# Kernel tuning notes

Hardware: AMD Instinct MI355X
Metric: run time of the kernel (lower is better)

The kernel has to match this reference:

```python
import jax, jax.numpy as jnp
import numpy as np

N = 50000          # num nodes
E = 800000         # num edges (before self loops)
DIM_IN = 128
HID = 32           # per-head hidden of conv1
HEADS = 8          # heads of conv1
DIM_OUT = 16       # output classes (conv2, 1 head, concat=False)
NEG_SLOPE = 0.2    # GATConv default leaky_relu slope


def gat_conv(x, W, a_src, a_dst, bias, src, dst, heads, out_ch, concat):
    """PyG GATConv (self-loops already appended to src/dst).
    x: [N, F_in], W: [F_in, heads*out_ch], a_src/a_dst: [heads, out_ch], bias matches output.
    """
    n = x.shape[0]
    h = (x @ W).reshape(n, heads, out_ch)                    # [N, H, C]
    al_src = jnp.einsum('nhc,hc->nh', h, a_src)              # [N, H]
    al_dst = jnp.einsum('nhc,hc->nh', h, a_dst)              # [N, H]
    e = jax.nn.leaky_relu(al_src[src] + al_dst[dst], NEG_SLOPE)   # [E', H]
    # segment softmax over edges grouped by target node (dst)
    emax = jax.ops.segment_max(e, dst, num_segments=n)       # [N, H]
    ee = jnp.exp(e - emax[dst])                              # [E', H]
    denom = jax.ops.segment_sum(ee, dst, num_segments=n)     # [N, H]
    alpha = ee / (denom[dst] + 1e-16)                        # [E', H]
    msg = h[src] * alpha[:, :, None]                         # [E', H, C]
    out = jax.ops.segment_sum(msg, dst, num_segments=n)      # [N, H, C]
    out = out.reshape(n, heads * out_ch) if concat else out.mean(axis=1)
    return out + bias


def setup_inputs() -> dict:
    key = jax.random.key(0)
    ks = jax.random.split(key, 12)
    x = jax.random.normal(ks[0], (N, DIM_IN), dtype=jnp.float32)
    edge_index = jax.random.randint(ks[1], (2, E), 0, N, dtype=jnp.int64)
    s = 0.1
    W1 = jax.random.normal(ks[2], (DIM_IN, HEADS * HID), dtype=jnp.float32) * s
    a1_src = jax.random.normal(ks[3], (HEADS, HID), dtype=jnp.float32) * s
    a1_dst = jax.random.normal(ks[4], (HEADS, HID), dtype=jnp.float32) * s
    b1 = jnp.zeros((HEADS * HID,), dtype=jnp.float32)
    W2 = jax.random.normal(ks[5], (HEADS * HID, DIM_OUT), dtype=jnp.float32) * s
    a2_src = jax.random.normal(ks[6], (1, DIM_OUT), dtype=jnp.float32) * s
    a2_dst = jax.random.normal(ks[7], (1, DIM_OUT), dtype=jnp.float32) * s
    b2 = jnp.zeros((DIM_OUT,), dtype=jnp.float32)
    return {"x": x, "edge_index": edge_index, "W1": W1, "a1_src": a1_src,
            "a1_dst": a1_dst, "b1": b1, "W2": W2, "a2_src": a2_src,
            "a2_dst": a2_dst, "b2": b2}


def reference(x, edge_index, W1, a1_src, a1_dst, b1, W2, a2_src, a2_dst, b2):
    # add self loops (GATConv default add_self_loops=True)
    loops = jnp.arange(N, dtype=edge_index.dtype)
    src = jnp.concatenate([edge_index[0], loops])
    dst = jnp.concatenate([edge_index[1], loops])
    # dropout layers are identity in eval mode
    h = gat_conv(x, W1, a1_src, a1_dst, b1, src, dst, HEADS, HID, concat=True)
    h = jax.nn.elu(h)
    out = gat_conv(h, W2, a2_src, a2_dst, b2, src, dst, 1, DIM_OUT, concat=False)
    return jax.nn.log_softmax(out, axis=1)
```

## Files before the change

kernel.cpp:

```cpp
#include <hip/hip_runtime.h>
#include <hip/hip_bf16.h>

#define NN 50000
#define EE 800000
#define EP (EE + NN)
#define DIN 128
#define HID 32
#define HEADS 8
#define C1 (HEADS * HID)
#define DOUT 16
#define NW1 3125
#define SH 9
#define NB 98
#define CAP 16384
#define EPT 8
#define BBLK (256 * EPT)
#define GB1 196

typedef __attribute__((ext_vector_type(8))) short short8;
typedef __attribute__((ext_vector_type(4))) float float4v;
typedef __attribute__((ext_vector_type(2))) float float2v;

__device__ inline unsigned short f2bf(float f) {
    __hip_bfloat16 b = __float2bfloat16(f);
    return *reinterpret_cast<unsigned short*>(&b);
}
__device__ inline float bflo(unsigned u) {
    union { unsigned int i; float f; } x;
    x.i = u << 16;
    return x.f;
}
__device__ inline float bfhi(unsigned u) {
    union { unsigned int i; float f; } x;
    x.i = u & 0xffff0000u;
    return x.f;
}
__device__ inline float bf2f(unsigned short u) {
    union { unsigned int i; float f; } x;
    x.i = ((unsigned int)u) << 16;
    return x.f;
}

__global__ void k_prepfw(const float* __restrict__ W1, const float* __restrict__ a1s,
                         const float* __restrict__ a1d, const float* __restrict__ W2,
                         unsigned short* __restrict__ w1frag,
                         unsigned short* __restrict__ w2frag,
                         int* __restrict__ cntb) {
    int i = blockIdx.x * 256 + threadIdx.x;
    if (blockIdx.x == 0 && threadIdx.x < NB) cntb[threadIdx.x] = 0;
    if (i < 17 * 2048) {
        int j = i & 7, lane = (i >> 3) & 63, s = (i >> 9) & 3, c = i >> 11;
        int q = lane >> 4, m = lane & 15;
        int k = s * 32 + q * 8 + j;
        float val;
        if (c < 16) {
            val = W1[k * C1 + c * 16 + m];
        } else {
            int h = m & 7;
            const float* av = (m < 8) ? a1s : a1d;
            float acc = 0.f;
            #pragma unroll
            for (int j2 = 0; j2 < 32; j2++)
                acc += W1[k * C1 + h * 32 + j2] * av[h * 32 + j2];
            val = acc;
        }
        w1frag[i] = f2bf(val);
    } else if (i < 17 * 2048 + 8 * 512) {
        int j2 = i - 17 * 2048;
        int jj = j2 & 7, lane = (j2 >> 3) & 63, s = j2 >> 9;
        int q = lane >> 4, m = lane & 15;
        w2frag[j2] = f2bf(W2[(s * 32 + q * 8 + jj) * DOUT + m]);
    }
}

__global__ __launch_bounds__(256) void k_bucketA(const int* __restrict__ ei,
                                                 int* __restrict__ cntb,
                                                 unsigned* __restrict__ ebuf) {
    __shared__ int hist[4][NB];
    __shared__ int base[4][NB];
    int t = threadIdx.x;
    int wave = t >> 6;
    for (int i = t; i < 4 * NB; i += 256) ((int*)hist)[i] = 0;
    __syncthreads();
    int e0 = blockIdx.x * BBLK;
    int s[EPT], d[EPT], r[EPT];
    #pragma unroll
    for (int j = 0; j < EPT; j++) {
        int e = e0 + j * 256 + t;
        int ss = 0, dd = -1;
        if (e < EE) { ss = ei[e]; dd = ei[EE + e]; }
        else if (e < EP) { ss = e - EE; dd = ss; }
        s[j] = ss; d[j] = dd;
        if (dd >= 0) r[j] = atomicAdd(&hist[wave][dd >> SH], 1);
    }
    __syncthreads();
    if (t < NB) {
        int h0 = hist[0][t], h1 = hist[1][t], h2 = hist[2][t], h3 = hist[3][t];
        int tot = h0 + h1 + h2 + h3;
        int bb = tot ? atomicAdd(&cntb[t], tot) : 0;
        base[0][t] = bb;
        base[1][t] = bb + h0;
        base[2][t] = bb + h0 + h1;
        base[3][t] = bb + h0 + h1 + h2;
    }
    __syncthreads();
    #pragma unroll
    for (int j = 0; j < EPT; j++) {
        if (d[j] >= 0) {
            int b = d[j] >> SH;
            ebuf[b * CAP + base[wave][b] + r[j]] =
                ((unsigned)s[j] << SH) | (unsigned)(d[j] & 511);
        }
    }
}

__global__ __launch_bounds__(1024) void k_csrgemm1(const int* __restrict__ cntb,
                                                   const unsigned* __restrict__ ebuf,
                                                   int* __restrict__ row_ptr,
                                                   int* __restrict__ esrc,
                                                   const float* __restrict__ x,
                                                   const unsigned short* __restrict__ w1frag,
                                                   unsigned char* __restrict__ h1f8,
                                                   float* __restrict__ al1sd,
                                                   unsigned short* __restrict__ al1s8) {
    __shared__ int sdeg[512];
    __shared__ int wtot[8];
    __shared__ int bpart[2];
    if (blockIdx.x < NB) {
        int b = blockIdx.x;
        int t = threadIdx.x;
        int lane = t & 63, wave = t >> 6;
        int nodes0 = b << SH;
        if (t < 512) sdeg[t] = 0;
        if (t < 128) {
            int v = (t < b) ? cntb[t] : 0;
            #pragma unroll
            for (int off = 1; off < 64; off <<= 1) v += __shfl_xor(v, off, 64);
            if (lane == 0) bpart[wave] = v;
        }
        __syncthreads();
        int baseS = bpart[0] + bpart[1];
        int cnt = cntb[b];
        const unsigned* eb = ebuf + b * CAP;
        for (int i = t; i < cnt; i += 1024)
            atomicAdd(&sdeg[eb[i] & 511], 1);
        __syncthreads();
        int v = (t < 512) ? sdeg[t] : 0;
        int inc = v;
        #pragma unroll
        for (int off = 1; off < 64; off <<= 1) {
            int u = __shfl_up(inc, off, 64);
            if (lane >= off) inc += u;
        }
        if (t < 512 && lane == 63) wtot[wave] = inc;
        __syncthreads();
        if (wave == 0 && lane < 8) {
            int w = wtot[lane];
            int iw = w;
            #pragma unroll
            for (int off = 1; off < 8; off <<= 1) {
                int u = __shfl_up(iw, off, 64);
                if (lane >= off) iw += u;
            }
            wtot[lane] = iw - w;
        }
        __syncthreads();
        int excl = inc - v + ((t < 512) ? wtot[wave] : 0);
        __syncthreads();
        if (t < 512) {
            sdeg[t] = excl;
            int node = nodes0 + t;
            if (node < NN) row_ptr[node] = baseS + excl;
        }
        __syncthreads();
        for (int i = t; i < cnt; i += 1024) {
            unsigned e = eb[i];
            int pos = atomicAdd(&sdeg[e & 511], 1);
            esrc[baseS + pos] = (int)(e >> SH);
        }
        if (b == 0 && t == 0) row_ptr[NN] = EP;
    } else {
        int wid = (blockIdx.x - NB) * 16 + (threadIdx.x >> 6);
        int lane = threadIdx.x & 63;
        if (wid >= NW1) return;
        int nb = wid * 16;
        int m = lane & 15, quad = lane >> 4;
        const float* xrow = x + (nb + m) * DIN;

        short8 bfr[4];
        #pragma unroll
        for (int s = 0; s < 4; s++) {
            float4 f0 = *(const float4*)(xrow + s * 32 + quad * 8);
            float4 f1 = *(const float4*)(xrow + s * 32 + quad * 8 + 4);
            unsigned short* bp = (unsigned short*)&bfr[s];
            bp[0] = f2bf(f0.x); bp[1] = f2bf(f0.y); bp[2] = f2bf(f0.z); bp[3] = f2bf(f0.w);
            bp[4] = f2bf(f1.x); bp[5] = f2bf(f1.y); bp[6] = f2bf(f1.z); bp[7] = f2bf(f1.w);
        }

        float4v acc[17];
        #pragma unroll
        for (int c = 0; c < 17; c++) acc[c] = (float4v){0.f, 0.f, 0.f, 0.f};

        #pragma unroll
        for (int s = 0; s < 4; s++) {
            const unsigned short* fp = w1frag + (s * 64 + lane) * 8;
            #pragma unroll
            for (int c = 0; c < 17; c++) {
                short8 afrag = *(const short8*)(fp + c * 2048);
                acc[c] = __builtin_amdgcn_mfma_f32_16x16x32_bf16(afrag, bfr[s], acc[c], 0, 0, 0);
            }
        }

        int node = nb + m;
        #pragma unroll
        for (int c = 0; c < 16; c++) {
            unsigned pk = 0;
            pk = __builtin_amdgcn_cvt_pk_fp8_f32(acc[c][0], acc[c][1], pk, false);
            pk = __builtin_amdgcn_cvt_pk_fp8_f32(acc[c][2], acc[c][3], pk, true);
            *(unsigned*)(h1f8 + node * C1 + c * 16 + quad * 4) = pk;
        }
        *(float4*)(al1sd + node * 16 + quad * 4) =
            make_float4(acc[16][0], acc[16][1], acc[16][2], acc[16][3]);
        if (quad < 2) {
            uint2 pk;
            pk.x = (unsigned)f2bf(acc[16][0]) | ((unsigned)f2bf(acc[16][1]) << 16);
            pk.y = (unsigned)f2bf(acc[16][2]) | ((unsigned)f2bf(acc[16][3]) << 16);
            *(uint2*)(al1s8 + node * 8 + quad * 4) = pk;
        }
    }
}

__global__ __launch_bounds__(256) void k_agg1(const int* __restrict__ row_ptr,
                                              const int* __restrict__ esrc,
                                              const unsigned char* __restrict__ h1f8,
                                              const unsigned short* __restrict__ al1s8,
                                              const float* __restrict__ al1sd,
                                              const float* __restrict__ b1,
                                              unsigned short* __restrict__ helu_b) {
    __shared__ float wbuf[4][64 * 8];
    __shared__ int   sbuf[4][64];
    int wslot = threadIdx.x >> 6;
    int L = threadIdx.x & 63;
    int d = (blockIdx.x * 256 + threadIdx.x) >> 6;
    int h = L >> 3;
    int start = row_ptr[d], end = row_ptr[d + 1];
    float4 ald0 = *(const float4*)(al1sd + d * 16 + 8);
    float4 ald1 = *(const float4*)(al1sd + d * 16 + 12);
    float* wrow = wbuf[wslot];
    int* srow = sbuf[wslot];
    float denom = 0.f;
    float4 acc = make_float4(0.f, 0.f, 0.f, 0.f);
    const int Lofs = L * 4;

    for (int base = start; base < end; base += 64) {
        int cnt = min(64, end - base);
        int s = d;
        float wv0 = 0.f, wv1 = 0.f, wv2 = 0.f, wv3 = 0.f;
        float wv4 = 0.f, wv5 = 0.f, wv6 = 0.f, wv7 = 0.f;
        if (L < cnt) {
            s = esrc[base + L];
            uint4 as = *(const uint4*)(al1s8 + s * 8);
            float e;
            e = bflo(as.x) + ald0.x; e = e > 0.f ? e : 0.2f * e; wv0 = __expf(e);
            e = bfhi(as.x) + ald0.y; e = e > 0.f ? e : 0.2f * e; wv1 = __expf(e);
            e = bflo(as.y) + ald0.z; e = e > 0.f ? e : 0.2f * e; wv2 = __expf(e);
            e = bfhi(as.y) + ald0.w; e = e > 0.f ? e : 0.2f * e; wv3 = __expf(e);
            e = bflo(as.z) + ald1.x; e = e > 0.f ? e : 0.2f * e; wv4 = __expf(e);
            e = bfhi(as.z) + ald1.y; e = e > 0.f ? e : 0.2f * e; wv5 = __expf(e);
            e = bflo(as.w) + ald1.z; e = e > 0.f ? e : 0.2f * e; wv6 = __expf(e);
            e = bfhi(as.w) + ald1.w; e = e > 0.f ? e : 0.2f * e; wv7 = __expf(e);
        }
        srow[L] = s;
        *(float4*)&wrow[L * 8]     = make_float4(wv0, wv1, wv2, wv3);
        *(float4*)&wrow[L * 8 + 4] = make_float4(wv4, wv5, wv6, wv7);
        int cnt4 = (cnt + 3) & ~3;
        for (int i = 0; i < cnt4; i += 4) {
            int s0 = srow[i], s1 = srow[i + 1], s2 = srow[i + 2], s3 = srow[i + 3];
            float x0 = wrow[i * 8 + h];
            float x1 = wrow[i * 8 + 8 + h];
            float x2 = wrow[i * 8 + 16 + h];
            float x3 = wrow[i * 8 + 24 + h];
            unsigned v0 = *(const unsigned*)(h1f8 + s0 * C1 + Lofs);
            unsigned v1 = *(const unsigned*)(h1f8 + s1 * C1 + Lofs);
            unsigned v2 = *(const unsigned*)(h1f8 + s2 * C1 + Lofs);
            unsigned v3 = *(const unsigned*)(h1f8 + s3 * C1 + Lofs);
            denom += (x0 + x1) + (x2 + x3);
            float2v a, b;
            a = __builtin_amdgcn_cvt_pk_f32_fp8(v0, false);
            b = __builtin_amdgcn_cvt_pk_f32_fp8(v0, true);
            acc.x += x0 * a.x; acc.y += x0 * a.y; acc.z += x0 * b.x; acc.w += x0 * b.y;
            a = __builtin_amdgcn_cvt_pk_f32_fp8(v1, false);
            b = __builtin_amdgcn_cvt_pk_f32_fp8(v1, true);
            acc.x += x1 * a.x; acc.y += x1 * a.y; acc.z += x1 * b.x; acc.w += x1 * b.y;
            a = __builtin_amdgcn_cvt_pk_f32_fp8(v2, false);
            b = __builtin_amdgcn_cvt_pk_f32_fp8(v2, true);
            acc.x += x2 * a.x; acc.y += x2 * a.y; acc.z += x2 * b.x; acc.w += x2 * b.y;
            a = __builtin_amdgcn_cvt_pk_f32_fp8(v3, false);
            b = __builtin_amdgcn_cvt_pk_f32_fp8(v3, true);
            acc.x += x3 * a.x; acc.y += x3 * a.y; acc.z += x3 * b.x; acc.w += x3 * b.y;
        }
    }
    float inv = 1.0f / (denom + 1e-16f);
    float4 bv = *(const float4*)(b1 + Lofs);
    float o0 = acc.x * inv + bv.x;
    float o1 = acc.y * inv + bv.y;
    float o2 = acc.z * inv + bv.z;
    float o3 = acc.w * inv + bv.w;
    o0 = o0 > 0.f ? o0 : __expf(o0) - 1.0f;
    o1 = o1 > 0.f ? o1 : __expf(o1) - 1.0f;
    o2 = o2 > 0.f ? o2 : __expf(o2) - 1.0f;
    o3 = o3 > 0.f ? o3 : __expf(o3) - 1.0f;
    uint2 pk;
    pk.x = (unsigned)f2bf(o0) | ((unsigned)f2bf(o1) << 16);
    pk.y = (unsigned)f2bf(o2) | ((unsigned)f2bf(o3) << 16);
    *(uint2*)(helu_b + d * C1 + Lofs) = pk;
}

__global__ __launch_bounds__(256) void k_gemm2(const unsigned short* __restrict__ helu_b,
                                               const unsigned short* __restrict__ w2frag,
                                               const float* __restrict__ a2s,
                                               const float* __restrict__ a2d,
                                               unsigned short* __restrict__ h2b,
                                               float* __restrict__ al2s,
                                               float* __restrict__ al2d) {
    int wid = (blockIdx.x * 256 + threadIdx.x) >> 6;
    int lane = threadIdx.x & 63;
    int nb = wid * 16;
    if (nb >= NN) return;
    int m = lane & 15, quad = lane >> 4;

    const unsigned short* wp2 = w2frag + lane * 8;
    float4v acc = {0.f, 0.f, 0.f, 0.f};
    const unsigned short* arow = helu_b + (nb + m) * C1 + quad * 8;
    #pragma unroll
    for (int s = 0; s < 8; s++) {
        short8 afrag = *(const short8*)(arow + s * 32);
        short8 bfrag = *(const short8*)(wp2 + s * 512);
        acc = __builtin_amdgcn_mfma_f32_16x16x32_bf16(afrag, bfrag, acc, 0, 0, 0);
    }

    float as_c = a2s[m], ad_c = a2d[m];
    #pragma unroll
    for (int r = 0; r < 4; r++) {
        int node = nb + quad * 4 + r;
        float val = acc[r];
        h2b[node * DOUT + m] = f2bf(val);
        float ps = val * as_c;
        float pd = val * ad_c;
        ps += __shfl_xor(ps, 1, 64); ps += __shfl_xor(ps, 2, 64);
        ps += __shfl_xor(ps, 4, 64); ps += __shfl_xor(ps, 8, 64);
        pd += __shfl_xor(pd, 1, 64); pd += __shfl_xor(pd, 2, 64);
        pd += __shfl_xor(pd, 4, 64); pd += __shfl_xor(pd, 8, 64);
        if (m == 0) {
            al2s[node] = ps;
            al2d[node] = pd;
        }
    }
}

__global__ __launch_bounds__(256) void k_agg2(const int* __restrict__ row_ptr,
                                              const int* __restrict__ esrc,
                                              const unsigned short* __restrict__ h2b,
                                              const float* __restrict__ al2s,
                                              const float* __restrict__ al2d,
                                              const float* __restrict__ b2,
                                              float* __restrict__ out) {
    __shared__ float wbuf2[4][64];
    __shared__ int   sbuf2[4][64];
    int wslot = threadIdx.x >> 6;
    int L = threadIdx.x & 63;
    int n = (blockIdx.x * 256 + threadIdx.x) >> 6;
    if (n >= NN) return;
    int c = L & 15, g = L >> 4;
    int start = row_ptr[n], end = row_ptr[n + 1];
    float ald = al2d[n];
    float* wrow = wbuf2[wslot];
    int* srow = sbuf2[wslot];
    float acc = 0.f, denom = 0.f;

    for (int base = start; base < end; base += 64) {
        int cnt = min(64, end - base);
        int s = n; float w = 0.f;
        if (L < cnt) {
            s = esrc[base + L];
            float e = al2s[s] + ald;
            e = e > 0.f ? e : 0.2f * e;
            w = __expf(e);
        }
        srow[L] = s;
        wrow[L] = w;
        int cnt4 = (cnt + 3) & ~3;
        for (int i = 0; i < cnt4; i += 4) {
            int idx = i + g;
            int ss = srow[idx];
            float ww = wrow[idx];
            float v = bf2f(h2b[ss * DOUT + c]);
            acc += ww * v;
            denom += ww;
        }
    }
    acc += __shfl_xor(acc, 16, 64);   acc += __shfl_xor(acc, 32, 64);
    denom += __shfl_xor(denom, 16, 64); denom += __shfl_xor(denom, 32, 64);
    float val = acc / (denom + 1e-16f) + b2[c];
    float m = val;
    #pragma unroll
    for (int mm = 1; mm < 16; mm <<= 1) m = fmaxf(m, __shfl_xor(m, mm, 64));
    float ex = __expf(val - m);
    float se = ex;
    #pragma unroll
    for (int mm = 1; mm < 16; mm <<= 1) se += __shfl_xor(se, mm, 64);
    if (L < 16) out[n * DOUT + c] = val - m - __logf(se);
}

extern "C" void kernel_launch(void* const* d_in, const int* in_sizes, int n_in,
                              void* d_out, int out_size, void* d_ws, size_t ws_size,
                              hipStream_t stream) {
    const float* x   = (const float*)d_in[0];
    const int*   ei  = (const int*)d_in[1];
    const float* W1  = (const float*)d_in[2];
    const float* a1s = (const float*)d_in[3];
    const float* a1d = (const float*)d_in[4];
    const float* b1  = (const float*)d_in[5];
    const float* W2  = (const float*)d_in[6];
    const float* a2s = (const float*)d_in[7];
    const float* a2d = (const float*)d_in[8];
    const float* b2  = (const float*)d_in[9];
    float* outp = (float*)d_out;

    unsigned char* h1f8    = (unsigned char*)d_ws;
    unsigned short* helu_b = (unsigned short*)(h1f8 + NN * C1);
    unsigned short* h2b    = helu_b + NN * C1;
    unsigned short* w2frag = h2b + NN * DOUT;
    unsigned short* w1frag = w2frag + 8 * 512;
    unsigned short* al1s8  = w1frag + 17 * 2048;
    float* al1sd = (float*)(al1s8 + NN * 8);
    float* al2sb = al1sd + NN * 16;
    float* al2db = al2sb + NN;
    int* row_ptr = (int*)(al2db + NN);
    int* esrc    = row_ptr + NN + 1;
    int* cntb    = esrc + EP;
    unsigned* ebuf = (unsigned*)helu_b;

    k_prepfw<<<(17 * 2048 + 8 * 512 + 255) / 256, 256, 0, stream>>>(W1, a1s, a1d, W2, w1frag, w2frag, cntb);
    k_bucketA<<<(EP + BBLK - 1) / BBLK, 256, 0, stream>>>(ei, cntb, ebuf);
    k_csrgemm1<<<NB + GB1, 1024, 0, stream>>>(cntb, ebuf, row_ptr, esrc,
                                              x, w1frag, h1f8, al1sd, al1s8);
    k_agg1<<<12500, 256, 0, stream>>>(row_ptr, esrc, h1f8, al1s8, al1sd, b1, helu_b);
    k_gemm2<<<(NW1 * 64 + 255) / 256, 256, 0, stream>>>(helu_b, w2frag, a2s, a2d, h2b, al2sb, al2db);
    k_agg2<<<(NN * 64 + 255) / 256, 256, 0, stream>>>(row_ptr, esrc, h2b, al2sb, al2db, b2, outp);
}
```

Baseline: 215.4 us.

## Split fused CSR/GEMM1 kernel and widen agg2 per-lane feature loads

Splits the combined CSR-build and first GEMM kernel into two launches: a 256-thread GEMM kernel with x loads hoisted ahead of the bf16 conversion, followed by a 1024-thread CSR kernel. This should give the GEMM better occupancy than it had inside 1024-thread blocks. In agg2, each lane now reads two bf16 features at once, so 8 edges are processed per iteration instead of 4, and the log-softmax uses one reciprocal and float2 stores. The cost is an extra kernel launch, and the CSR and GEMM phases can no longer run at the same time within one grid.

```diff
diff --git a/kernel.cpp b/kernel.cpp
--- a/kernel.cpp
+++ b/kernel.cpp
@@ -15,7 +15,6 @@
 #define CAP 16384
 #define EPT 8
 #define BBLK (256 * EPT)
-#define GB1 196
 
 typedef __attribute__((ext_vector_type(8))) short short8;
 typedef __attribute__((ext_vector_type(4))) float float4v;
@@ -114,119 +113,123 @@
     }
 }
 
-__global__ __launch_bounds__(1024) void k_csrgemm1(const int* __restrict__ cntb,
-                                                   const unsigned* __restrict__ ebuf,
-                                                   int* __restrict__ row_ptr,
-                                                   int* __restrict__ esrc,
-                                                   const float* __restrict__ x,
-                                                   const unsigned short* __restrict__ w1frag,
-                                                   unsigned char* __restrict__ h1f8,
-                                                   float* __restrict__ al1sd,
-                                                   unsigned short* __restrict__ al1s8) {
+__global__ __launch_bounds__(1024) void k_csr(const int* __restrict__ cntb,
+                                              const unsigned* __restrict__ ebuf,
+                                              int* __restrict__ row_ptr,
+                                              int* __restrict__ esrc) {
     __shared__ int sdeg[512];
     __shared__ int wtot[8];
     __shared__ int bpart[2];
-    if (blockIdx.x < NB) {
-        int b = blockIdx.x;
-        int t = threadIdx.x;
-        int lane = t & 63, wave = t >> 6;
-        int nodes0 = b << SH;
-        if (t < 512) sdeg[t] = 0;
-        if (t < 128) {
-            int v = (t < b) ? cntb[t] : 0;
-            #pragma unroll
-            for (int off = 1; off < 64; off <<= 1) v += __shfl_xor(v, off, 64);
-            if (lane == 0) bpart[wave] = v;
-        }
-        __syncthreads();
-        int baseS = bpart[0] + bpart[1];
-        int cnt = cntb[b];
-        const unsigned* eb = ebuf + b * CAP;
-        for (int i = t; i < cnt; i += 1024)
-            atomicAdd(&sdeg[eb[i] & 511], 1);
-        __syncthreads();
-        int v = (t < 512) ? sdeg[t] : 0;
-        int inc = v;
+    int b = blockIdx.x;
+    int t = threadIdx.x;
+    int lane = t & 63, wave = t >> 6;
+    int nodes0 = b << SH;
+    if (t < 512) sdeg[t] = 0;
+    if (t < 128) {
+        int v = (t < b) ? cntb[t] : 0;
         #pragma unroll
-        for (int off = 1; off < 64; off <<= 1) {
-            int u = __shfl_up(inc, off, 64);
-            if (lane >= off) inc += u;
-        }
-        if (t < 512 && lane == 63) wtot[wave] = inc;
-        __syncthreads();
-        if (wave == 0 && lane < 8) {
-            int w = wtot[lane];
-            int iw = w;
-            #pragma unroll
-            for (int off = 1; off < 8; off <<= 1) {
-                int u = __shfl_up(iw, off, 64);
-                if (lane >= off) iw += u;
-            }
-            wtot[lane] = iw - w;
-        }
-        __syncthreads();
-        int excl = inc - v + ((t < 512) ? wtot[wave] : 0);
-        __syncthreads();
-        if (t < 512) {
-            sdeg[t] = excl;
-            int node = nodes0 + t;
-            if (node < NN) row_ptr[node] = baseS + excl;
-        }
-        __syncthreads();
-        for (int i = t; i < cnt; i += 1024) {
-            unsigned e = eb[i];
-            int pos = atomicAdd(&sdeg[e & 511], 1);
-            esrc[baseS + pos] = (int)(e >> SH);
-        }
-        if (b == 0 && t == 0) row_ptr[NN] = EP;
-    } else {
-        int wid = (blockIdx.x - NB) * 16 + (threadIdx.x >> 6);
-        int lane = threadIdx.x & 63;
-        if (wid >= NW1) return;
-        int nb = wid * 16;
-        int m = lane & 15, quad = lane >> 4;
-        const float* xrow = x + (nb + m) * DIN;
-
-        short8 bfr[4];
+        for (int off = 1; off < 64; off <<= 1) v += __shfl_xor(v, off, 64);
+        if (lane == 0) bpart[wave] = v;
+    }
+    __syncthreads();
+    int baseS = bpart[0] + bpart[1];
+    int cnt = cntb[b];
+    const unsigned* eb = ebuf + b * CAP;
+    for (int i = t; i < cnt; i += 1024)
+        atomicAdd(&sdeg[eb[i] & 511], 1);
+    __syncthreads();
+    int v = (t < 512) ? sdeg[t] : 0;
+    int inc = v;
+    #pragma unroll
+    for (int off = 1; off < 64; off <<= 1) {
+        int u = __shfl_up(inc, off, 64);
+        if (lane >= off) inc += u;
+    }
+    if (t < 512 && lane == 63) wtot[wave] = inc;
+    __syncthreads();
+    if (wave == 0 && lane < 8) {
+        int w = wtot[lane];
+        int iw = w;
         #pragma unroll
-        for (int s = 0; s < 4; s++) {
-            float4 f0 = *(const float4*)(xrow + s * 32 + quad * 8);
-            float4 f1 = *(const float4*)(xrow + s * 32 + quad * 8 + 4);
-            unsigned short* bp = (unsigned short*)&bfr[s];
-            bp[0] = f2bf(f0.x); bp[1] = f2bf(f0.y); bp[2] = f2bf(f0.z); bp[3] = f2bf(f0.w);
-            bp[4] = f2bf(f1.x); bp[5] = f2bf(f1.y); bp[6] = f2bf(f1.z); bp[7] = f2bf(f1.w);
-        }
-
-        float4v acc[17];
+        for (int off = 1; off < 8; off <<= 1) {
+            int u = __shfl_up(iw, off, 64);
+            if (lane >= off) iw += u;
+        }
+        wtot[lane] = iw - w;
+    }
+    __syncthreads();
+    int excl = inc - v + ((t < 512) ? wtot[wave] : 0);
+    __syncthreads();
+    if (t < 512) {
+        sdeg[t] = excl;
+        int node = nodes0 + t;
+        if (node < NN) row_ptr[node] = baseS + excl;
+    }
+    __syncthreads();
+    for (int i = t; i < cnt; i += 1024) {
+        unsigned e = eb[i];
+        int pos = atomicAdd(&sdeg[e & 511], 1);
+        esrc[baseS + pos] = (int)(e >> SH);
+    }
+    if (b == 0 && t == 0) row_ptr[NN] = EP;
+}
+
+__global__ __launch_bounds__(256) void k_gemm1(const float* __restrict__ x,
+                                               const unsigned short* __restrict__ w1frag,
+                                               unsigned char* __restrict__ h1f8,
+                                               float* __restrict__ al1sd,
+                                               unsigned short* __restrict__ al1s8) {
+    int wid = (blockIdx.x * 256 + threadIdx.x) >> 6;
+    int lane = threadIdx.x & 63;
+    if (wid >= NW1) return;
+    int nb = wid * 16;
+    int m = lane & 15, quad = lane >> 4;
+    const float* xrow = x + (nb + m) * DIN;
+
+    float4 xf[8];
+    #pragma unroll
+    for (int s = 0; s < 4; s++) {
+        xf[2 * s]     = *(const float4*)(xrow + s * 32 + quad * 8);
+        xf[2 * s + 1] = *(const float4*)(xrow + s * 32 + quad * 8 + 4);
+    }
+    short8 bfr[4];
+    #pragma unroll
+    for (int s = 0; s < 4; s++) {
+        unsigned short* bp = (unsigned short*)&bfr[s];
+        float4 f0 = xf[2 * s], f1 = xf[2 * s + 1];
+        bp[0] = f2bf(f0.x); bp[1] = f2bf(f0.y); bp[2] = f2bf(f0.z); bp[3] = f2bf(f0.w);
+        bp[4] = f2bf(f1.x); bp[5] = f2bf(f1.y); bp[6] = f2bf(f1.z); bp[7] = f2bf(f1.w);
+    }
+
+    float4v acc[17];
+    #pragma unroll
+    for (int c = 0; c < 17; c++) acc[c] = (float4v){0.f, 0.f, 0.f, 0.f};
+
+    #pragma unroll
+    for (int s = 0; s < 4; s++) {
+        const unsigned short* fp = w1frag + (s * 64 + lane) * 8;
         #pragma unroll
-        for (int c = 0; c < 17; c++) acc[c] = (float4v){0.f, 0.f, 0.f, 0.f};
-
-        #pragma unroll
-        for (int s = 0; s < 4; s++) {
-            const unsigned short* fp = w1frag + (s * 64 + lane) * 8;
-            #pragma unroll
-            for (int c = 0; c < 17; c++) {
-                short8 afrag = *(const short8*)(fp + c * 2048);
-                acc[c] = __builtin_amdgcn_mfma_f32_16x16x32_bf16(afrag, bfr[s], acc[c], 0, 0, 0);
-            }
-        }
-
-        int node = nb + m;
-        #pragma unroll
-        for (int c = 0; c < 16; c++) {
-            unsigned pk = 0;
-            pk = __builtin_amdgcn_cvt_pk_fp8_f32(acc[c][0], acc[c][1], pk, false);
-            pk = __builtin_amdgcn_cvt_pk_fp8_f32(acc[c][2], acc[c][3], pk, true);
-            *(unsigned*)(h1f8 + node * C1 + c * 16 + quad * 4) = pk;
-        }
-        *(float4*)(al1sd + node * 16 + quad * 4) =
-            make_float4(acc[16][0], acc[16][1], acc[16][2], acc[16][3]);
-        if (quad < 2) {
-            uint2 pk;
-            pk.x = (unsigned)f2bf(acc[16][0]) | ((unsigned)f2bf(acc[16][1]) << 16);
-            pk.y = (unsigned)f2bf(acc[16][2]) | ((unsigned)f2bf(acc[16][3]) << 16);
-            *(uint2*)(al1s8 + node * 8 + quad * 4) = pk;
-        }
+        for (int c = 0; c < 17; c++) {
+            short8 afrag = *(const short8*)(fp + c * 2048);
+            acc[c] = __builtin_amdgcn_mfma_f32_16x16x32_bf16(afrag, bfr[s], acc[c], 0, 0, 0);
+        }
+    }
+
+    int node = nb + m;
+    #pragma unroll
+    for (int c = 0; c < 16; c++) {
+        unsigned pk = 0;
+        pk = __builtin_amdgcn_cvt_pk_fp8_f32(acc[c][0], acc[c][1], pk, false);
+        pk = __builtin_amdgcn_cvt_pk_fp8_f32(acc[c][2], acc[c][3], pk, true);
+        *(unsigned*)(h1f8 + node * C1 + c * 16 + quad * 4) = pk;
+    }
+    *(float4*)(al1sd + node * 16 + quad * 4) =
+        make_float4(acc[16][0], acc[16][1], acc[16][2], acc[16][3]);
+    if (quad < 2) {
+        uint2 pk;
+        pk.x = (unsigned)f2bf(acc[16][0]) | ((unsigned)f2bf(acc[16][1]) << 16);
+        pk.y = (unsigned)f2bf(acc[16][2]) | ((unsigned)f2bf(acc[16][3]) << 16);
+        *(uint2*)(al1s8 + node * 8 + quad * 4) = pk;
     }
 }
 
@@ -371,12 +374,12 @@
     int L = threadIdx.x & 63;
     int n = (blockIdx.x * 256 + threadIdx.x) >> 6;
     if (n >= NN) return;
-    int c = L & 15, g = L >> 4;
+    int p = L & 7, g = L >> 3;
     int start = row_ptr[n], end = row_ptr[n + 1];
     float ald = al2d[n];
     float* wrow = wbuf2[wslot];
     int* srow = sbuf2[wslot];
-    float acc = 0.f, denom = 0.f;
+    float acc0 = 0.f, acc1 = 0.f, denom = 0.f;
 
     for (int base = start; base < end; base += 64) {
         int cnt = min(64, end - base);
@@ -389,27 +392,35 @@
         }
         srow[L] = s;
         wrow[L] = w;
-        int cnt4 = (cnt + 3) & ~3;
-        for (int i = 0; i < cnt4; i += 4) {
+        int cnt8 = (cnt + 7) & ~7;
+        for (int i = 0; i < cnt8; i += 8) {
             int idx = i + g;
             int ss = srow[idx];
             float ww = wrow[idx];
-            float v = bf2f(h2b[ss * DOUT + c]);
-            acc += ww * v;
+            unsigned v = *(const unsigned*)(h2b + ss * DOUT + p * 2);
+            acc0 += ww * bflo(v);
+            acc1 += ww * bfhi(v);
             denom += ww;
         }
     }
-    acc += __shfl_xor(acc, 16, 64);   acc += __shfl_xor(acc, 32, 64);
-    denom += __shfl_xor(denom, 16, 64); denom += __shfl_xor(denom, 32, 64);
-    float val = acc / (denom + 1e-16f) + b2[c];
-    float m = val;
-    #pragma unroll
-    for (int mm = 1; mm < 16; mm <<= 1) m = fmaxf(m, __shfl_xor(m, mm, 64));
-    float ex = __expf(val - m);
-    float se = ex;
-    #pragma unroll
-    for (int mm = 1; mm < 16; mm <<= 1) se += __shfl_xor(se, mm, 64);
-    if (L < 16) out[n * DOUT + c] = val - m - __logf(se);
+    acc0 += __shfl_xor(acc0, 8, 64);  acc0 += __shfl_xor(acc0, 16, 64);  acc0 += __shfl_xor(acc0, 32, 64);
+    acc1 += __shfl_xor(acc1, 8, 64);  acc1 += __shfl_xor(acc1, 16, 64);  acc1 += __shfl_xor(acc1, 32, 64);
+    denom += __shfl_xor(denom, 8, 64); denom += __shfl_xor(denom, 16, 64); denom += __shfl_xor(denom, 32, 64);
+    float inv = 1.0f / (denom + 1e-16f);
+    float2 bv = *(const float2*)(b2 + p * 2);
+    float val0 = acc0 * inv + bv.x;
+    float val1 = acc1 * inv + bv.y;
+    float m = fmaxf(val0, val1);
+    #pragma unroll
+    for (int mm = 1; mm < 8; mm <<= 1) m = fmaxf(m, __shfl_xor(m, mm, 64));
+    float se = __expf(val0 - m) + __expf(val1 - m);
+    #pragma unroll
+    for (int mm = 1; mm < 8; mm <<= 1) se += __shfl_xor(se, mm, 64);
+    float lse = m + __logf(se);
+    if (L < 8) {
+        float2 o = make_float2(val0 - lse, val1 - lse);
+        *(float2*)(out + n * DOUT + p * 2) = o;
+    }
 }
 
 extern "C" void kernel_launch(void* const* d_in, const int* in_sizes, int n_in,
@@ -443,8 +454,8 @@
 
     k_prepfw<<<(17 * 2048 + 8 * 512 + 255) / 256, 256, 0, stream>>>(W1, a1s, a1d, W2, w1frag, w2frag, cntb);
     k_bucketA<<<(EP + BBLK - 1) / BBLK, 256, 0, stream>>>(ei, cntb, ebuf);
-    k_csrgemm1<<<NB + GB1, 1024, 0, stream>>>(cntb, ebuf, row_ptr, esrc,
-                                              x, w1frag, h1f8, al1sd, al1s8);
+    k_gemm1<<<(NW1 * 64 + 255) / 256, 256, 0, stream>>>(x, w1frag, h1f8, al1sd, al1s8);
+    k_csr<<<NB, 1024, 0, stream>>>(cntb, ebuf, row_ptr, esrc);
     k_agg1<<<12500, 256, 0, stream>>>(row_ptr, esrc, h1f8, al1s8, al1sd, b1, helu_b);
     k_gemm2<<<(NW1 * 64 + 255) / 256, 256, 0, stream>>>(helu_b, w2frag, a2s, a2d, h2b, al2sb, al2db);
     k_agg2<<<(NN * 64 + 255) / 256, 256, 0, stream>>>(row_ptr, esrc, h2b, al2sb, al2db, b2, outp);
```

After: 205.3 us. 1.05x faster.
